# Performance work log

Measured on AMD Instinct MI355X. Metric: run time of the kernel, lower is better.

The kernel has to match this reference:

```python
import jax, jax.numpy as jnp
import numpy as np

B, N, L, S = 32, 100000, 12, 256
SIGMA = 1.0          # gaussian filter sigma (pixels)
PIXEL = 1.0          # sampling rate (A/px)
LAMBDA = 0.0197      # electron wavelength at 300 kV (A)
CS = 2.7e7           # spherical aberration (A)
Q0 = 0.1             # amplitude contrast


def setup_inputs() -> dict:
    key = jax.random.key(0)
    ks = jax.random.split(key, 10)
    return {
        "c_nma": jax.random.normal(ks[0], (B, L), jnp.float32),
        "delta_euler": 0.1 * jax.random.normal(ks[1], (B, 3), jnp.float32),
        "delta_shifts": jax.random.normal(ks[2], (B, 2), jnp.float32),
        "coords": (jax.random.uniform(ks[3], (N, 3), jnp.float32) - 0.5) * (S / 2.0),
        "basis_x": 0.01 * jax.random.normal(ks[4], (N, L), jnp.float32),
        "basis_y": 0.01 * jax.random.normal(ks[5], (N, L), jnp.float32),
        "basis_z": 0.01 * jax.random.normal(ks[6], (N, L), jnp.float32),
        "euler_base": 2.0 * np.pi * jax.random.uniform(ks[7], (B, 3), jnp.float32),
        "shifts_base": 2.0 * jax.random.normal(ks[8], (B, 2), jnp.float32),
        "defocus": 1e4 + 1.5e4 * jax.random.uniform(ks[9], (B,), jnp.float32),
    }


def _euler_to_rot(eu):
    # ZYZ (xmipp) convention: rot, tilt, psi -> [B,3,3]
    rot, tilt, psi = eu[..., 0], eu[..., 1], eu[..., 2]
    ca, sa = jnp.cos(rot), jnp.sin(rot)
    cb, sb = jnp.cos(tilt), jnp.sin(tilt)
    cg, sg = jnp.cos(psi), jnp.sin(psi)
    r0 = jnp.stack([cg * cb * ca - sg * sa, cg * cb * sa + sg * ca, -cg * sb], -1)
    r1 = jnp.stack([-sg * cb * ca - cg * sa, -sg * cb * sa + cg * ca, sg * sb], -1)
    r2 = jnp.stack([sb * ca, sb * sa, cb], -1)
    return jnp.stack([r0, r1, r2], -2)


def _forward(c_nma, delta_euler, delta_shifts, coords, basis_x, basis_y, basis_z,
             euler_base, shifts_base, defocus):
    # deformation field + apply: [B,N]
    c_x = coords[:, 0][None, :] + jnp.einsum('bl,nl->bn', c_nma, basis_x)
    c_y = coords[:, 1][None, :] + jnp.einsum('bl,nl->bn', c_nma, basis_y)
    c_z = coords[:, 2][None, :] + jnp.einsum('bl,nl->bn', c_nma, basis_z)
    p = jnp.stack([c_x, c_y, c_z], -1)               # [B,N,3]

    # bond lengths between consecutive atoms: [B,N-1]
    dvec = p[:, 1:] - p[:, :-1]
    bondk = jnp.sqrt(jnp.sum(dvec * dvec, -1) + 1e-12)
    # angles at interior atoms: [B,N-2]
    u = p[:, :-2] - p[:, 1:-1]
    v = p[:, 2:] - p[:, 1:-1]
    cosang = jnp.sum(u * v, -1) / (
        jnp.sqrt(jnp.sum(u * u, -1)) * jnp.sqrt(jnp.sum(v * v, -1)) + 1e-12)
    anglek = jnp.arccos(jnp.clip(cosang, -0.9999, 0.9999))

    # alignment with refined euler angles, keep x/y projection rows: [B,N,2]
    R = _euler_to_rot(euler_base + delta_euler)
    proj = jnp.einsum('bij,bnj->bni', R[:, :2], p)
    sh = shifts_base + delta_shifts
    x = proj[..., 0] + sh[:, 0:1] + S / 2.0
    y = proj[..., 1] + sh[:, 1:2] + S / 2.0

    # bilinear scatter-add splat into [B,S,S]
    x = jnp.clip(x, 0.0, S - 1.001)
    y = jnp.clip(y, 0.0, S - 1.001)
    x0 = jnp.floor(x).astype(jnp.int32); fx = x - x0
    y0 = jnp.floor(y).astype(jnp.int32); fy = y - y0
    x1, y1 = x0 + 1, y0 + 1
    b_idx = jnp.arange(B, dtype=jnp.int32)[:, None]
    flat = lambda xi, yi: ((b_idx * S + yi) * S + xi).ravel()
    idx = jnp.concatenate([flat(x0, y0), flat(x1, y0), flat(x0, y1), flat(x1, y1)])
    w = jnp.concatenate([((1 - fx) * (1 - fy)).ravel(), (fx * (1 - fy)).ravel(),
                         ((1 - fx) * fy).ravel(), (fx * fy).ravel()])
    img = jnp.zeros(B * S * S, x.dtype).at[idx].add(w).reshape(B, S, S)

    # gaussian low-pass + CTF in Fourier space
    freq_y = jnp.fft.fftfreq(S).astype(x.dtype)
    freq_x = jnp.fft.rfftfreq(S).astype(x.dtype)
    s2 = freq_y[:, None] ** 2 + freq_x[None, :] ** 2          # [S, S//2+1]
    G = jnp.exp(-2.0 * (jnp.pi * SIGMA) ** 2 * s2)
    F = jnp.fft.rfft2(img) * G
    s2a = s2 / (PIXEL ** 2)
    chi = (jnp.pi * LAMBDA * defocus[:, None, None] * s2a
           - 0.5 * jnp.pi * CS * LAMBDA ** 3 * s2a ** 2)
    ctf = -(jnp.sqrt(1.0 - Q0 ** 2) * jnp.sin(chi) + Q0 * jnp.cos(chi))
    decoded = jnp.fft.irfft2(F * ctf, s=(S, S))
    return decoded, bondk, anglek


def reference(c_nma, delta_euler, delta_shifts, coords, basis_x, basis_y, basis_z,
              euler_base, shifts_base, defocus):
    return _forward(c_nma, delta_euler, delta_shifts, coords, basis_x, basis_y,
                    basis_z, euler_base, shifts_base, defocus)
```

## Files before the change

kernel.cpp:

```cpp
#include <hip/hip_runtime.h>
#include <math.h>

namespace {
constexpr int kB = 32;
constexpr int kN = 100000;
constexpr int kL = 12;
constexpr int kS = 256;
constexpr int kBG = 8;
constexpr int kWOwn = 62;
constexpr int kTile = 4 * kWOwn;
constexpr int kNB = (kN + kTile - 1) / kTile;
constexpr int kCap = 16384;
constexpr int kKx = 130;
constexpr int kGPad = 16;

constexpr float kGauss = (float)(2.0 * M_PI * M_PI);
constexpr float kA1 = (float)(M_PI * 0.0197);
constexpr float kA2 = (float)(0.5 * M_PI * 2.7e7 * 0.0197 * 0.0197 * 0.0197);
constexpr float kW1 = 0.99498743710661995f;
constexpr float kQ0 = 0.1f;
}

__global__ __launch_bounds__(256) void k_zero(int* __restrict__ gcount) {
  const int t = threadIdx.x;
#pragma unroll
  for (int i = 0; i < kB * 8 * kGPad / 256; ++i) gcount[i * 256 + t] = 0;
}

__device__ __forceinline__ void build_tw(float2* tw, int t) {
  if (t < 128) {
    float s, c;
    sincosf((float)M_PI / 128.0f * (float)t, &s, &c);
    tw[t] = make_float2(c, s);
  }
}

template <int SIGN>
__device__ __forceinline__ void fft256w(float2 v[4], float2* fb, int lane,
                                        const float2* tw) {
#pragma unroll
  for (int m = 1; m <= 64; m *= 4) {
    int l = lane & (m - 1);
    int jm = lane - l;
    float2 wv = tw[jm];
    float c = wv.x;
    float s = (SIGN < 0) ? -wv.y : wv.y;
    float2 A0 = v[0], A1 = v[1], A2 = v[2], A3 = v[3];
    float s02x = A0.x + A2.x, s02y = A0.y + A2.y;
    float d02x = A0.x - A2.x, d02y = A0.y - A2.y;
    float s13x = A1.x + A3.x, s13y = A1.y + A3.y;
    float d13x = A1.x - A3.x, d13y = A1.y - A3.y;
    float jdx = (SIGN < 0) ? d13y : -d13y;
    float jdy = (SIGN < 0) ? -d13x : d13x;
    float t1x = d02x + jdx, t1y = d02y + jdy;
    float t2x = s02x - s13x, t2y = s02y - s13y;
    float t3x = d02x - jdx, t3y = d02y - jdy;
    float c2 = c * c - s * s, s2 = 2.f * c * s;
    float c3 = c2 * c - s2 * s, s3 = c2 * s + s2 * c;
    int ob = 4 * jm + l;
    fb[ob]         = make_float2(s02x + s13x, s02y + s13y);
    fb[ob + m]     = make_float2(c * t1x - s * t1y, c * t1y + s * t1x);
    fb[ob + 2 * m] = make_float2(c2 * t2x - s2 * t2y, c2 * t2y + s2 * t2x);
    fb[ob + 3 * m] = make_float2(c3 * t3x - s3 * t3y, c3 * t3y + s3 * t3x);
    v[0] = fb[lane];
    v[1] = fb[lane + 64];
    v[2] = fb[lane + 128];
    v[3] = fb[lane + 192];
  }
}

__global__ __launch_bounds__(256) void k_deform(
    const float* __restrict__ c_nma, const float* __restrict__ delta_euler,
    const float* __restrict__ delta_shifts, const float* __restrict__ coords,
    const float* __restrict__ basis_x, const float* __restrict__ basis_y,
    const float* __restrict__ basis_z, const float* __restrict__ euler_base,
    const float* __restrict__ shifts_base,
    unsigned* __restrict__ xy_bkt, int* __restrict__ gcount,
    float* __restrict__ bond, float* __restrict__ angle) {
  __shared__ float cn_s[kBG][kL];
  __shared__ float rsh_s[kBG][8];
  __shared__ int bcnt[kBG][8];
  __shared__ int bbase[kBG][8];

  const int t = threadIdx.x;
  const int wave = t >> 6, lane = t & 63;
  const int bg = blockIdx.y * kBG;
  const int n = blockIdx.x * kTile + wave * kWOwn + lane;
  const bool owner = (lane < kWOwn) && (n < kN);
  const int nc = min(n, kN - 1);

  if (t < kBG * kL) cn_s[t / kL][t % kL] = c_nma[(bg + t / kL) * kL + (t % kL)];
  if (t < kBG) {
    int b = bg + t;
    float rot  = euler_base[b * 3 + 0] + delta_euler[b * 3 + 0];
    float tilt = euler_base[b * 3 + 1] + delta_euler[b * 3 + 1];
    float psi  = euler_base[b * 3 + 2] + delta_euler[b * 3 + 2];
    float ca = cosf(rot), sa = sinf(rot);
    float cb = cosf(tilt), sb = sinf(tilt);
    float cg = cosf(psi), sg = sinf(psi);
    rsh_s[t][0] = cg * cb * ca - sg * sa;
    rsh_s[t][1] = cg * cb * sa + sg * ca;
    rsh_s[t][2] = -cg * sb;
    rsh_s[t][3] = -sg * cb * ca - cg * sa;
    rsh_s[t][4] = -sg * cb * sa + cg * ca;
    rsh_s[t][5] = sg * sb;
    rsh_s[t][6] = shifts_base[b * 2 + 0] + delta_shifts[b * 2 + 0] + 128.0f;
    rsh_s[t][7] = shifts_base[b * 2 + 1] + delta_shifts[b * 2 + 1] + 128.0f;
  }
  if (t < kBG * 8) bcnt[t >> 3][t & 7] = 0;

  const float cx = coords[nc * 3 + 0];
  const float cy = coords[nc * 3 + 1];
  const float cz = coords[nc * 3 + 2];
  float bx[kL], by[kL], bz[kL];
  {
    const float4* px4 = reinterpret_cast<const float4*>(basis_x + (size_t)nc * kL);
    const float4* py4 = reinterpret_cast<const float4*>(basis_y + (size_t)nc * kL);
    const float4* pz4 = reinterpret_cast<const float4*>(basis_z + (size_t)nc * kL);
#pragma unroll
    for (int q = 0; q < 3; ++q) {
      float4 vx = px4[q], vy = py4[q], vz = pz4[q];
      bx[q * 4 + 0] = vx.x; bx[q * 4 + 1] = vx.y; bx[q * 4 + 2] = vx.z; bx[q * 4 + 3] = vx.w;
      by[q * 4 + 0] = vy.x; by[q * 4 + 1] = vy.y; by[q * 4 + 2] = vy.z; by[q * 4 + 3] = vy.w;
      bz[q * 4 + 0] = vz.x; bz[q * 4 + 1] = vz.y; bz[q * 4 + 2] = vz.z; bz[q * 4 + 3] = vz.w;
    }
  }
  __syncthreads();

  unsigned ureg[kBG];
  unsigned meta[kBG];
  unsigned meta2[kBG];

#pragma unroll
  for (int bi = 0; bi < kBG; ++bi) {
    const int b = bg + bi;
    float px = cx, py = cy, pz = cz;
#pragma unroll
    for (int l = 0; l < kL; ++l) {
      float cc = cn_s[bi][l];
      px = fmaf(cc, bx[l], px);
      py = fmaf(cc, by[l], py);
      pz = fmaf(cc, bz[l], pz);
    }
    float p1x = __shfl_down(px, 1), p1y = __shfl_down(py, 1), p1z = __shfl_down(pz, 1);
    float dx = p1x - px, dy = p1y - py, dz = p1z - pz;
    float dd = fmaf(dx, dx, fmaf(dy, dy, dz * dz));
    float d1x = __shfl_down(dx, 1), d1y = __shfl_down(dy, 1), d1z = __shfl_down(dz, 1);

    ureg[bi] = 0; meta[bi] = 0; meta2[bi] = ~0u;
    if (owner) {
      float xr = fmaf(rsh_s[bi][0], px, fmaf(rsh_s[bi][1], py, fmaf(rsh_s[bi][2], pz, rsh_s[bi][6])));
      float yr = fmaf(rsh_s[bi][3], px, fmaf(rsh_s[bi][4], py, fmaf(rsh_s[bi][5], pz, rsh_s[bi][7])));
      xr = fminf(fmaxf(xr, 0.0f), 254.999f);
      yr = fminf(fmaxf(yr, 0.0f), 254.999f);
      unsigned xf = (unsigned)(xr * 256.0f);
      unsigned yf = (unsigned)(yr * 256.0f);
      unsigned y0i = yf >> 8;
      unsigned band = y0i >> 5;
      int rank = atomicAdd(&bcnt[bi][band], 1);
      ureg[bi] = (yf << 16) | xf;
      meta[bi] = ((unsigned)rank << 3) | band;
      if ((y0i & 31u) == 31u) {
        unsigned band1 = band + 1;
        int r2 = atomicAdd(&bcnt[bi][band1], 1);
        meta2[bi] = ((unsigned)r2 << 3) | band1;
      }
      if (n < kN - 1) {
        __builtin_nontemporal_store(sqrtf(dd + 1e-12f),
                                    &bond[(size_t)b * (kN - 1) + n]);
      }
      if (n < kN - 2) {
        float vv = fmaf(d1x, d1x, fmaf(d1y, d1y, d1z * d1z));
        float uv = -fmaf(dx, d1x, fmaf(dy, d1y, dz * d1z));
        float cosang = uv * rsqrtf(dd * vv);
        cosang = fminf(fmaxf(cosang, -0.9999f), 0.9999f);
        float ax = fabsf(cosang);
        float rt = sqrtf(1.0f - ax);
        float pp = fmaf(fmaf(fmaf(-0.0187293f, ax, 0.0742610f), ax, -0.2121144f),
                        ax, 1.5707288f);
        float res = rt * pp;
        __builtin_nontemporal_store((cosang >= 0.f) ? res : (float)M_PI - res,
                                    &angle[(size_t)b * (kN - 2) + n]);
      }
    }
  }
  __syncthreads();
  if (t < kBG * 8) {
    int po = t >> 3, bandx = t & 7;
    int c = bcnt[po][bandx];
    bbase[po][bandx] =
        c ? atomicAdd(&gcount[((bg + po) * 8 + bandx) * kGPad], c) : 0;
  }
  __syncthreads();
#pragma unroll
  for (int bi = 0; bi < kBG; ++bi) {
    if (owner) {
      unsigned band = meta[bi] & 7;
      int pos = bbase[bi][band] + (int)(meta[bi] >> 3);
      if (pos < kCap) xy_bkt[((size_t)(bg + bi) * 8 + band) * kCap + pos] = ureg[bi];
      if (meta2[bi] != ~0u) {
        unsigned band1 = meta2[bi] & 7;
        int pos2 = bbase[bi][band1] + (int)(meta2[bi] >> 3);
        if (pos2 < kCap)
          xy_bkt[((size_t)(bg + bi) * 8 + band1) * kCap + pos2] = ureg[bi];
      }
    }
  }
}

__global__ __launch_bounds__(1024) void k_splat_fft(
    const unsigned* __restrict__ xy_bkt, const int* __restrict__ gcount,
    float2* __restrict__ FcT) {
  __shared__ unsigned tile[32 * 256];
  __shared__ float2 fbuf[16][256];
  __shared__ float2 tw[128];
  const int t = threadIdx.x;
  const int b = blockIdx.x >> 3;
  const int band = blockIdx.x & 7;
  const int r0 = band * 32;
  build_tw(tw, t);
  for (int i = t; i < 32 * 256; i += 1024) tile[i] = 0u;
  __syncthreads();

  const int c = min(gcount[(b * 8 + band) * kGPad], kCap);
  const unsigned* seg = xy_bkt + ((size_t)b * 8 + band) * kCap;

  auto splat1 = [&](unsigned u) {
    int yf = (int)(u >> 16);
    int xf = (int)(u & 0xFFFFu);
    int ry = (yf >> 8) - r0;
    int x0 = xf >> 8;
    int fx = xf & 255, fy = yf & 255;
    int gx = 256 - fx, gy = 256 - fy;
    if ((unsigned)ry < 32u) {
      int base = ry * 256 + x0;
      atomicAdd(&tile[base],     (unsigned)((gx * gy + 2) >> 2));
      atomicAdd(&tile[base + 1], (unsigned)((fx * gy + 2) >> 2));
    }
    if ((unsigned)(ry + 1) < 32u) {
      int base = (ry + 1) * 256 + x0;
      atomicAdd(&tile[base],     (unsigned)((gx * fy + 2) >> 2));
      atomicAdd(&tile[base + 1], (unsigned)((fx * fy + 2) >> 2));
    }
  };

  const int c4 = c & ~3;
  const uint4* seg4 = reinterpret_cast<const uint4*>(seg);
  for (int i4 = t; i4 * 4 < c4; i4 += 1024) {
    uint4 q = seg4[i4];
    splat1(q.x); splat1(q.y); splat1(q.z); splat1(q.w);
  }
  for (int i = c4 + t; i < c; i += 1024) splat1(seg[i]);
  __syncthreads();

  const int w = t >> 6, lane = t & 63;
  const int rowA = 2 * w;
  constexpr float scale = 1.0f / 16384.0f;
  float2 v[4];
#pragma unroll
  for (int j = 0; j < 4; ++j) {
    int i = lane + 64 * j;
    v[j] = make_float2((float)tile[rowA * 256 + i] * scale,
                       (float)tile[(rowA + 1) * 256 + i] * scale);
  }
  fft256w<-1>(v, fbuf[w], lane, tw);
  float2* a = fbuf[w];
  const int y = r0 + rowA;
#pragma unroll
  for (int j = 0; j < 2; ++j) {
    int k = lane + 64 * j;
    float2 Zk = a[k], Zm = a[(256 - k) & 255];
    float4 o = make_float4(0.5f * (Zk.x + Zm.x), 0.5f * (Zk.y - Zm.y),
                           0.5f * (Zk.y + Zm.y), 0.5f * (Zm.x - Zk.x));
    *reinterpret_cast<float4*>(&FcT[((size_t)b * kKx + k) * kS + y]) = o;
  }
  if (lane == 0) {
    float2 Zk = a[128];
    *reinterpret_cast<float4*>(&FcT[((size_t)b * kKx + 128) * kS + y]) =
        make_float4(Zk.x, 0.f, Zk.y, 0.f);
  }
}

__global__ __launch_bounds__(256) void k_fft_cols(float2* __restrict__ FcT,
                                                  const float* __restrict__ defocus) {
  __shared__ float2 fbuf[4][256];
  __shared__ float2 tw[128];
  const int t = threadIdx.x, w = t >> 6, lane = t & 63;
  build_tw(tw, t);
  const int b = blockIdx.x / 33;
  const int kx = (blockIdx.x % 33) * 4 + w;
  __syncthreads();
  if (kx > 128) return;
  float2* col = FcT + ((size_t)b * kKx + kx) * kS;
  float2 v[4];
#pragma unroll
  for (int j = 0; j < 4; ++j) v[j] = col[lane + 64 * j];
  fft256w<-1>(v, fbuf[w], lane, tw);

  const float D = defocus[b];
  const float fxv = (float)kx * (1.0f / 256.0f);
  const float fx2 = fxv * fxv;
#pragma unroll
  for (int j = 0; j < 4; ++j) {
    int ky = lane + 64 * j;
    float fyv = (float)(ky < 128 ? ky : ky - 256) * (1.0f / 256.0f);
    float s2 = fyv * fyv + fx2;
    float G = __expf(-kGauss * s2);
    float chi = kA1 * D * s2 - kA2 * s2 * s2;
    float sn, cn;
    sincosf(chi, &sn, &cn);
    float H = G * (-(kW1 * sn + kQ0 * cn));
    v[j].x *= H;
    v[j].y *= H;
  }
  fft256w<1>(v, fbuf[w], lane, tw);
#pragma unroll
  for (int j = 0; j < 4; ++j) col[lane + 64 * j] = v[j];
}

__global__ __launch_bounds__(256) void k_fft_rows_inv(const float2* __restrict__ FcT,
                                                      float* __restrict__ out) {
  __shared__ float2 fbuf[4][256];
  __shared__ float4 smT[4][132];
  __shared__ float2 tw[128];
  const int t = threadIdx.x, w = t >> 6, lane = t & 63;
  build_tw(tw, t);
  const int b = blockIdx.x >> 5;
  const int pp = (blockIdx.x & 31) * 4 + w;
  const int y = 2 * pp;

  const float4* Fp = reinterpret_cast<const float4*>(FcT + (size_t)b * kKx * kS + y);
  const size_t kstep = kS / 2;
  smT[w][lane]      = Fp[(size_t)lane * kstep];
  smT[w][lane + 64] = Fp[(size_t)(lane + 64) * kstep];
  if (lane == 0) smT[w][128] = Fp[(size_t)128 * kstep];
  __syncthreads();

  float2 v[4];
  {
    float4 f = smT[w][lane];
    v[0] = make_float2(f.x - f.w, f.y + f.z);
  }
  {
    float4 f = smT[w][lane + 64];
    v[1] = make_float2(f.x - f.w, f.y + f.z);
  }
  if (lane == 0) {
    float4 f = smT[w][128];
    v[2] = make_float2(f.x - f.w, f.y + f.z);
  } else {
    float4 f = smT[w][128 - lane];
    v[2] = make_float2(f.x + f.w, -f.y + f.z);
  }
  {
    float4 f = smT[w][64 - lane];
    v[3] = make_float2(f.x + f.w, -f.y + f.z);
  }
  fft256w<1>(v, fbuf[w], lane, tw);

  float* o0 = out + ((size_t)b * kS + y) * kS;
  float* o1 = o0 + kS;
#pragma unroll
  for (int j = 0; j < 4; ++j) {
    int i = lane + 64 * j;
    o0[i] = v[j].x * (1.0f / 65536.0f);
    o1[i] = v[j].y * (1.0f / 65536.0f);
  }
}

extern "C" void kernel_launch(void* const* d_in, const int* in_sizes, int n_in,
                              void* d_out, int out_size, void* d_ws, size_t ws_size,
                              hipStream_t stream) {
  const float* c_nma        = (const float*)d_in[0];
  const float* delta_euler  = (const float*)d_in[1];
  const float* delta_shifts = (const float*)d_in[2];
  const float* coords       = (const float*)d_in[3];
  const float* basis_x      = (const float*)d_in[4];
  const float* basis_y      = (const float*)d_in[5];
  const float* basis_z      = (const float*)d_in[6];
  const float* euler_base   = (const float*)d_in[7];
  const float* shifts_base  = (const float*)d_in[8];
  const float* defocus      = (const float*)d_in[9];

  float* out = (float*)d_out;
  float* decoded = out;
  float* bond    = out + (size_t)kB * kS * kS;
  float* angle   = bond + (size_t)kB * (kN - 1);

  char* ws = (char*)d_ws;
  unsigned* xy_bkt = (unsigned*)ws;
  float2*   FcT    = (float2*)(ws + (size_t)16 * 1024 * 1024);
  int*      gcount = (int*)(ws + (size_t)25 * 1024 * 1024);

  k_zero<<<1, 256, 0, stream>>>(gcount);

  dim3 gd(kNB, kB / kBG);
  k_deform<<<gd, 256, 0, stream>>>(c_nma, delta_euler, delta_shifts, coords,
                                   basis_x, basis_y, basis_z, euler_base,
                                   shifts_base, xy_bkt, gcount, bond, angle);
  k_splat_fft<<<kB * 8, 1024, 0, stream>>>(xy_bkt, gcount, FcT);
  k_fft_cols<<<kB * 33, 256, 0, stream>>>(FcT, defocus);
  k_fft_rows_inv<<<kB * 32, 256, 0, stream>>>(FcT, decoded);
}
```

Baseline: 65.80 us.

## Replace global atomic bucket allocation with fixed per-block slots for splat lists

Each deform block now writes its projected atom coordinates straight into a fixed 64-entry slot per (batch, band, block) and records a per-block count. Before, blocks reserved space in shared per-band buckets through a global atomic and then ran a second scatter pass. This removes the global atomics, the second scatter pass and the separate zeroing kernel launch. The splat kernel then walks all per-block slots, one wave per slot. The risk is that bands receiving more than 64 atoms from one block silently drop atoms, and the splat kernel must read every slot even when it is sparse.

Result: faster. 57.35 us (-12.8%).

```diff
diff --git a/kernel.cpp b/kernel.cpp
--- a/kernel.cpp
+++ b/kernel.cpp
@@ -10,21 +10,14 @@
 constexpr int kWOwn = 62;
 constexpr int kTile = 4 * kWOwn;
 constexpr int kNB = (kN + kTile - 1) / kTile;
-constexpr int kCap = 16384;
+constexpr int kSlot = 64;
 constexpr int kKx = 130;
-constexpr int kGPad = 16;
 
 constexpr float kGauss = (float)(2.0 * M_PI * M_PI);
 constexpr float kA1 = (float)(M_PI * 0.0197);
 constexpr float kA2 = (float)(0.5 * M_PI * 2.7e7 * 0.0197 * 0.0197 * 0.0197);
 constexpr float kW1 = 0.99498743710661995f;
 constexpr float kQ0 = 0.1f;
-}
-
-__global__ __launch_bounds__(256) void k_zero(int* __restrict__ gcount) {
-  const int t = threadIdx.x;
-#pragma unroll
-  for (int i = 0; i < kB * 8 * kGPad / 256; ++i) gcount[i * 256 + t] = 0;
 }
 
 __device__ __forceinline__ void build_tw(float2* tw, int t) {
@@ -75,17 +68,17 @@
     const float* __restrict__ basis_x, const float* __restrict__ basis_y,
     const float* __restrict__ basis_z, const float* __restrict__ euler_base,
     const float* __restrict__ shifts_base,
-    unsigned* __restrict__ xy_bkt, int* __restrict__ gcount,
+    unsigned* __restrict__ xy_bkt, int* __restrict__ cnt,
     float* __restrict__ bond, float* __restrict__ angle) {
   __shared__ float cn_s[kBG][kL];
   __shared__ float rsh_s[kBG][8];
   __shared__ int bcnt[kBG][8];
-  __shared__ int bbase[kBG][8];
 
   const int t = threadIdx.x;
   const int wave = t >> 6, lane = t & 63;
   const int bg = blockIdx.y * kBG;
-  const int n = blockIdx.x * kTile + wave * kWOwn + lane;
+  const int xb = blockIdx.x;
+  const int n = xb * kTile + wave * kWOwn + lane;
   const bool owner = (lane < kWOwn) && (n < kN);
   const int nc = min(n, kN - 1);
 
@@ -127,10 +120,6 @@
   }
   __syncthreads();
 
-  unsigned ureg[kBG];
-  unsigned meta[kBG];
-  unsigned meta2[kBG];
-
 #pragma unroll
   for (int bi = 0; bi < kBG; ++bi) {
     const int b = bg + bi;
@@ -147,7 +136,6 @@
     float dd = fmaf(dx, dx, fmaf(dy, dy, dz * dz));
     float d1x = __shfl_down(dx, 1), d1y = __shfl_down(dy, 1), d1z = __shfl_down(dz, 1);
 
-    ureg[bi] = 0; meta[bi] = 0; meta2[bi] = ~0u;
     if (owner) {
       float xr = fmaf(rsh_s[bi][0], px, fmaf(rsh_s[bi][1], py, fmaf(rsh_s[bi][2], pz, rsh_s[bi][6])));
       float yr = fmaf(rsh_s[bi][3], px, fmaf(rsh_s[bi][4], py, fmaf(rsh_s[bi][5], pz, rsh_s[bi][7])));
@@ -155,15 +143,17 @@
       yr = fminf(fmaxf(yr, 0.0f), 254.999f);
       unsigned xf = (unsigned)(xr * 256.0f);
       unsigned yf = (unsigned)(yr * 256.0f);
+      unsigned u = (yf << 16) | xf;
       unsigned y0i = yf >> 8;
       unsigned band = y0i >> 5;
       int rank = atomicAdd(&bcnt[bi][band], 1);
-      ureg[bi] = (yf << 16) | xf;
-      meta[bi] = ((unsigned)rank << 3) | band;
+      if (rank < kSlot)
+        xy_bkt[(((size_t)b * 8 + band) * kNB + xb) * kSlot + rank] = u;
       if ((y0i & 31u) == 31u) {
         unsigned band1 = band + 1;
         int r2 = atomicAdd(&bcnt[bi][band1], 1);
-        meta2[bi] = ((unsigned)r2 << 3) | band1;
+        if (r2 < kSlot)
+          xy_bkt[(((size_t)b * 8 + band1) * kNB + xb) * kSlot + r2] = u;
       }
       if (n < kN - 1) {
         __builtin_nontemporal_store(sqrtf(dd + 1e-12f),
@@ -187,43 +177,28 @@
   __syncthreads();
   if (t < kBG * 8) {
     int po = t >> 3, bandx = t & 7;
-    int c = bcnt[po][bandx];
-    bbase[po][bandx] =
-        c ? atomicAdd(&gcount[((bg + po) * 8 + bandx) * kGPad], c) : 0;
-  }
-  __syncthreads();
-#pragma unroll
-  for (int bi = 0; bi < kBG; ++bi) {
-    if (owner) {
-      unsigned band = meta[bi] & 7;
-      int pos = bbase[bi][band] + (int)(meta[bi] >> 3);
-      if (pos < kCap) xy_bkt[((size_t)(bg + bi) * 8 + band) * kCap + pos] = ureg[bi];
-      if (meta2[bi] != ~0u) {
-        unsigned band1 = meta2[bi] & 7;
-        int pos2 = bbase[bi][band1] + (int)(meta2[bi] >> 3);
-        if (pos2 < kCap)
-          xy_bkt[((size_t)(bg + bi) * 8 + band1) * kCap + pos2] = ureg[bi];
-      }
-    }
+    cnt[((bg + po) * 8 + bandx) * kNB + xb] = min(bcnt[po][bandx], kSlot);
   }
 }
 
 __global__ __launch_bounds__(1024) void k_splat_fft(
-    const unsigned* __restrict__ xy_bkt, const int* __restrict__ gcount,
+    const unsigned* __restrict__ xy_bkt, const int* __restrict__ cnt,
     float2* __restrict__ FcT) {
   __shared__ unsigned tile[32 * 256];
   __shared__ float2 fbuf[16][256];
   __shared__ float2 tw[128];
+  __shared__ int cnt_s[kNB];
   const int t = threadIdx.x;
   const int b = blockIdx.x >> 3;
   const int band = blockIdx.x & 7;
   const int r0 = band * 32;
   build_tw(tw, t);
   for (int i = t; i < 32 * 256; i += 1024) tile[i] = 0u;
-  __syncthreads();
-
-  const int c = min(gcount[(b * 8 + band) * kGPad], kCap);
-  const unsigned* seg = xy_bkt + ((size_t)b * 8 + band) * kCap;
+  for (int i = t; i < kNB; i += 1024) cnt_s[i] = cnt[(b * 8 + band) * kNB + i];
+  __syncthreads();
+
+  const int w = t >> 6, lane = t & 63;
+  const unsigned* segbase = xy_bkt + ((size_t)b * 8 + band) * kNB * kSlot;
 
   auto splat1 = [&](unsigned u) {
     int yf = (int)(u >> 16);
@@ -244,16 +219,13 @@
     }
   };
 
-  const int c4 = c & ~3;
-  const uint4* seg4 = reinterpret_cast<const uint4*>(seg);
-  for (int i4 = t; i4 * 4 < c4; i4 += 1024) {
-    uint4 q = seg4[i4];
-    splat1(q.x); splat1(q.y); splat1(q.z); splat1(q.w);
-  }
-  for (int i = c4 + t; i < c; i += 1024) splat1(seg[i]);
-  __syncthreads();
-
-  const int w = t >> 6, lane = t & 63;
+  for (int j = w; j < kNB; j += 16) {
+    int cc = cnt_s[j];
+    unsigned u = segbase[(size_t)j * kSlot + lane];
+    if (lane < cc) splat1(u);
+  }
+  __syncthreads();
+
   const int rowA = 2 * w;
   constexpr float scale = 1.0f / 16384.0f;
   float2 v[4];
@@ -388,17 +360,16 @@
   float* angle   = bond + (size_t)kB * (kN - 1);
 
   char* ws = (char*)d_ws;
+  const size_t bktBytes = (size_t)kB * 8 * kNB * kSlot * sizeof(unsigned);
   unsigned* xy_bkt = (unsigned*)ws;
-  float2*   FcT    = (float2*)(ws + (size_t)16 * 1024 * 1024);
-  int*      gcount = (int*)(ws + (size_t)25 * 1024 * 1024);
-
-  k_zero<<<1, 256, 0, stream>>>(gcount);
+  int*      cnt    = (int*)(ws + bktBytes);
+  float2*   FcT    = (float2*)(ws + (size_t)28 * 1024 * 1024);
 
   dim3 gd(kNB, kB / kBG);
   k_deform<<<gd, 256, 0, stream>>>(c_nma, delta_euler, delta_shifts, coords,
                                    basis_x, basis_y, basis_z, euler_base,
-                                   shifts_base, xy_bkt, gcount, bond, angle);
-  k_splat_fft<<<kB * 8, 1024, 0, stream>>>(xy_bkt, gcount, FcT);
+                                   shifts_base, xy_bkt, cnt, bond, angle);
+  k_splat_fft<<<kB * 8, 1024, 0, stream>>>(xy_bkt, cnt, FcT);
   k_fft_cols<<<kB * 33, 256, 0, stream>>>(FcT, defocus);
   k_fft_rows_inv<<<kB * 32, 256, 0, stream>>>(FcT, decoded);
 }
```
